# Performance work log

Measured on AMD Instinct MI355X. Metric: run time of the kernel, lower is better.

Reference implementation:

```python
import jax, jax.numpy as jnp
import numpy as np

UP_TIME = 1440.0
UP_DIST = 40.0
LOC_CNT = 100000
LOC_LEN = 131072
H = 256


def setup_inputs() -> dict:
    key = jax.random.key(0)
    ks = jax.random.split(key, 12)
    stdv = 1.0 / np.sqrt(H)
    u = lambda k, shape: jax.random.uniform(k, shape, jnp.float32, -stdv, stdv)
    return {
        "td_upper": jax.random.uniform(ks[0], (LOC_LEN,), jnp.float32),
        "td_lower": jax.random.uniform(ks[1], (LOC_LEN,), jnp.float32),
        "ld_upper": jax.random.uniform(ks[2], (LOC_LEN,), jnp.float32),
        "ld_lower": jax.random.uniform(ks[3], (LOC_LEN,), jnp.float32),
        "loc": jax.random.randint(ks[4], (LOC_LEN,), 0, LOC_CNT, jnp.int32),
        "hx": jax.random.normal(ks[5], (H, 1), jnp.float32),
        "weight_ih": u(ks[6], (H, H)),
        "weight_th_upper": u(ks[7], (H, H)),
        "weight_th_lower": u(ks[8], (H, H)),
        "weight_sh_upper": u(ks[9], (H, H)),
        "weight_sh_lower": u(ks[10], (H, H)),
        "location_weight": u(ks[11], (LOC_CNT, H)),
    }


def reference(td_upper, td_lower, ld_upper, ld_lower, loc, hx,
              weight_ih, weight_th_upper, weight_th_lower,
              weight_sh_upper, weight_sh_lower, location_weight):
    tu = jnp.clip(td_upper, 0.0, UP_TIME)
    tl = jnp.clip(td_lower, 0.0, UP_TIME)
    lu = jnp.clip(ld_upper, 0.0, UP_DIST)
    ll = jnp.clip(ld_lower, 0.0, UP_DIST)

    e = location_weight[loc]  # [L, H] gathered POI embeddings
    # Ttd[i] @ e[i] = (tu[i]*W_tu@e[i] + tl[i]*W_tl@e[i]) / (tu[i]+tl[i])
    a = jnp.einsum('hk,lk->lh', weight_th_upper, e)
    b = jnp.einsum('hk,lk->lh', weight_th_lower, e)
    t = (tu[:, None] * a + tl[:, None] * b) / (tu + tl)[:, None]  # [L, H]
    # Sld[i] @ t[i]
    c = jnp.einsum('hk,lk->lh', weight_sh_upper, t)
    d = jnp.einsum('hk,lk->lh', weight_sh_lower, t)
    s = (lu[:, None] * c + ll[:, None] * d) / (lu + ll)[:, None]  # [L, H]

    loc_vec = jnp.sum(s, axis=0)[:, None]  # [H, 1]
    usr_vec = weight_ih @ hx               # [H, 1]
    return jax.nn.sigmoid(loc_vec + usr_vec)
```

## Files before the change

### kernel.cpp

```cpp
#include <hip/hip_runtime.h>
#include <math.h>

#define H 256
#define TILE 256

__global__ __launch_bounds__(256) void strnn_gather(
    const float* __restrict__ td_u, const float* __restrict__ td_l,
    const float* __restrict__ ld_u, const float* __restrict__ ld_l,
    const int* __restrict__ loc, const float* __restrict__ table,
    float* __restrict__ v, int L)
{
    __shared__ float4 s_w[TILE];
    __shared__ int    s_loc[TILE];
    __shared__ float  s_red[4][4][H];
    const int t    = threadIdx.x;
    const int wave = t >> 6;
    const int lane = t & 63;

    float4 a0 = {0,0,0,0}, a1 = {0,0,0,0}, a2 = {0,0,0,0}, a3 = {0,0,0,0};

    for (int base = blockIdx.x * TILE; base < L; base += gridDim.x * TILE) {
        const int l = base + t;
        const bool ok = (l < L);
        float tu = ok ? fminf(fmaxf(td_u[l], 0.f), 1440.f) : 1.f;
        float tl = ok ? fminf(fmaxf(td_l[l], 0.f), 1440.f) : 1.f;
        float lu = ok ? fminf(fmaxf(ld_u[l], 0.f), 40.f)   : 1.f;
        float ll = ok ? fminf(fmaxf(ld_l[l], 0.f), 40.f)   : 1.f;
        float al = tu / (tu + tl);
        float be = lu / (lu + ll);
        float w0 = be * al, w1 = be * (1.f - al);
        float w2 = (1.f - be) * al, w3 = (1.f - be) * (1.f - al);
        if (!ok) { w0 = w1 = w2 = w3 = 0.f; }
        s_w[t]   = make_float4(w0, w1, w2, w3);
        s_loc[t] = ok ? loc[l] : 0;
        __syncthreads();

        const int r0 = wave * 64;
        #pragma unroll 2
        for (int j = 0; j < 64; j += 8) {
            const float4* addr[8];
            #pragma unroll
            for (int u = 0; u < 8; ++u)
                addr[u] = (const float4*)(table + (size_t)s_loc[r0 + j + u] * H + 4 * lane);
            float4 w[8], e[8];
            #pragma unroll
            for (int u = 0; u < 8; ++u)
                e[u] = *addr[u];
            #pragma unroll
            for (int u = 0; u < 8; ++u)
                w[u] = s_w[r0 + j + u];
            #pragma unroll
            for (int u = 0; u < 8; ++u) {
                a0.x = fmaf(w[u].x, e[u].x, a0.x);
                a0.y = fmaf(w[u].x, e[u].y, a0.y);
                a0.z = fmaf(w[u].x, e[u].z, a0.z);
                a0.w = fmaf(w[u].x, e[u].w, a0.w);
                a1.x = fmaf(w[u].y, e[u].x, a1.x);
                a1.y = fmaf(w[u].y, e[u].y, a1.y);
                a1.z = fmaf(w[u].y, e[u].z, a1.z);
                a1.w = fmaf(w[u].y, e[u].w, a1.w);
                a2.x = fmaf(w[u].z, e[u].x, a2.x);
                a2.y = fmaf(w[u].z, e[u].y, a2.y);
                a2.z = fmaf(w[u].z, e[u].z, a2.z);
                a2.w = fmaf(w[u].z, e[u].w, a2.w);
                a3.x = fmaf(w[u].w, e[u].x, a3.x);
                a3.y = fmaf(w[u].w, e[u].y, a3.y);
                a3.z = fmaf(w[u].w, e[u].z, a3.z);
                a3.w = fmaf(w[u].w, e[u].w, a3.w);
            }
        }
        __syncthreads();
    }

    *(float4*)&s_red[wave][0][4 * lane] = a0;
    *(float4*)&s_red[wave][1][4 * lane] = a1;
    *(float4*)&s_red[wave][2][4 * lane] = a2;
    *(float4*)&s_red[wave][3][4 * lane] = a3;
    __syncthreads();
    #pragma unroll
    for (int c = 0; c < 4; ++c) {
        float s = s_red[0][c][t] + s_red[1][c][t] + s_red[2][c][t] + s_red[3][c][t];
        atomicAdd(&v[c * H + t], s);
    }
}

__global__ __launch_bounds__(256) void strnn_mid(
    const float* __restrict__ Wtu, const float* __restrict__ Wtl,
    const float* __restrict__ Wih, const float* __restrict__ hx,
    const float* __restrict__ v, float* __restrict__ pqu)
{
    const int wave = (blockIdx.x * blockDim.x + threadIdx.x) >> 6;
    const int lane = threadIdx.x & 63;
    const float* v1 = v;
    const float* v2 = v + H;
    const float* v3 = v + 2 * H;
    const float* v4 = v + 3 * H;

    float p = 0.f, q = 0.f, u = 0.f;
    #pragma unroll
    for (int i = 0; i < H; i += 64) {
        const int k = i + lane;
        const float wtu = Wtu[wave * H + k];
        const float wtl = Wtl[wave * H + k];
        p = fmaf(wtu, v1[k], fmaf(wtl, v2[k], p));
        q = fmaf(wtu, v3[k], fmaf(wtl, v4[k], q));
        u = fmaf(Wih[wave * H + k], hx[k], u);
    }
    #pragma unroll
    for (int off = 32; off > 0; off >>= 1) {
        p += __shfl_down(p, off, 64);
        q += __shfl_down(q, off, 64);
        u += __shfl_down(u, off, 64);
    }
    if (lane == 0) {
        pqu[wave]         = p;
        pqu[H + wave]     = q;
        pqu[2 * H + wave] = u;
    }
}

__global__ __launch_bounds__(256) void strnn_out(
    const float* __restrict__ Wsu, const float* __restrict__ Wsl,
    const float* __restrict__ pqu, float* __restrict__ out)
{
    const int wave = (blockIdx.x * blockDim.x + threadIdx.x) >> 6;
    const int lane = threadIdx.x & 63;
    const float* p = pqu;
    const float* q = pqu + H;
    const float* u = pqu + 2 * H;

    float s = 0.f;
    #pragma unroll
    for (int i = 0; i < H; i += 64) {
        const int k = i + lane;
        s = fmaf(Wsu[wave * H + k], p[k], fmaf(Wsl[wave * H + k], q[k], s));
    }
    #pragma unroll
    for (int off = 32; off > 0; off >>= 1)
        s += __shfl_down(s, off, 64);
    if (lane == 0)
        out[wave] = 1.f / (1.f + expf(-(s + u[wave])));
}

extern "C" void kernel_launch(void* const* d_in, const int* in_sizes, int n_in,
                              void* d_out, int out_size, void* d_ws, size_t ws_size,
                              hipStream_t stream) {
    const float* td_u  = (const float*)d_in[0];
    const float* td_l  = (const float*)d_in[1];
    const float* ld_u  = (const float*)d_in[2];
    const float* ld_l  = (const float*)d_in[3];
    const int*   loc   = (const int*)d_in[4];
    const float* hx    = (const float*)d_in[5];
    const float* Wih   = (const float*)d_in[6];
    const float* Wtu   = (const float*)d_in[7];
    const float* Wtl   = (const float*)d_in[8];
    const float* Wsu   = (const float*)d_in[9];
    const float* Wsl   = (const float*)d_in[10];
    const float* table = (const float*)d_in[11];
    const int L = in_sizes[0];

    float* v   = (float*)d_ws;
    float* pqu = v + 4 * H;

    hipMemsetAsync(v, 0, 4 * H * sizeof(float), stream);

    strnn_gather<<<512, 256, 0, stream>>>(td_u, td_l, ld_u, ld_l, loc, table, v, L);
    strnn_mid<<<64, 256, 0, stream>>>(Wtu, Wtl, Wih, hx, v, pqu);
    strnn_out<<<64, 256, 0, stream>>>(Wsu, Wsl, pqu, (float*)d_out);
}
```

Measured before the change: 183.4 us.

## Aggregate per-location weights by scatter, then stream the table in row order

Samples that share a location index are now merged first. A scatter kernel atomically accumulates the four mixing coefficients per sample into a per-location weight buffer. A second kernel then walks the embedding table in row order and accumulates weighted rows. Rows with zero total weight are redirected to row 0, so their distinct loads are skipped. This turns many random 1KB row gathers, including repeats, into near-sequential reads of the touched rows. In exchange it adds a larger workspace memset, contended atomics and an extra kernel launch, and it changes the float summation order.

```diff
diff --git a/kernel.cpp b/kernel.cpp
--- a/kernel.cpp
+++ b/kernel.cpp
@@ -2,74 +2,88 @@
 #include <math.h>
 
 #define H 256
-#define TILE 256
 
-__global__ __launch_bounds__(256) void strnn_gather(
+__global__ __launch_bounds__(256) void strnn_scatter(
     const float* __restrict__ td_u, const float* __restrict__ td_l,
     const float* __restrict__ ld_u, const float* __restrict__ ld_l,
-    const int* __restrict__ loc, const float* __restrict__ table,
-    float* __restrict__ v, int L)
+    const int* __restrict__ loc, float* __restrict__ W, int L)
 {
-    __shared__ float4 s_w[TILE];
-    __shared__ int    s_loc[TILE];
-    __shared__ float  s_red[4][4][H];
+    const int i = blockIdx.x * 256 + threadIdx.x;
+    if (i >= L) return;
+    float tu = fminf(fmaxf(td_u[i], 0.f), 1440.f);
+    float tl = fminf(fmaxf(td_l[i], 0.f), 1440.f);
+    float lu = fminf(fmaxf(ld_u[i], 0.f), 40.f);
+    float ll = fminf(fmaxf(ld_l[i], 0.f), 40.f);
+    float al = tu / (tu + tl);
+    float be = lu / (lu + ll);
+    float* w = W + 4 * (size_t)loc[i];
+    atomicAdd(w + 0, be * al);
+    atomicAdd(w + 1, be * (1.f - al));
+    atomicAdd(w + 2, (1.f - be) * al);
+    atomicAdd(w + 3, (1.f - be) * (1.f - al));
+}
+
+__global__ __launch_bounds__(256) void strnn_stream(
+    const float* __restrict__ table, const float* __restrict__ W,
+    float* __restrict__ v, int R)
+{
+    __shared__ float s_red[4][4][H];
     const int t    = threadIdx.x;
     const int wave = t >> 6;
     const int lane = t & 63;
+    const int gw   = blockIdx.x * 4 + wave;
+    const int nw   = gridDim.x * 4;
 
     float4 a0 = {0,0,0,0}, a1 = {0,0,0,0}, a2 = {0,0,0,0}, a3 = {0,0,0,0};
 
-    for (int base = blockIdx.x * TILE; base < L; base += gridDim.x * TILE) {
-        const int l = base + t;
-        const bool ok = (l < L);
-        float tu = ok ? fminf(fmaxf(td_u[l], 0.f), 1440.f) : 1.f;
-        float tl = ok ? fminf(fmaxf(td_l[l], 0.f), 1440.f) : 1.f;
-        float lu = ok ? fminf(fmaxf(ld_u[l], 0.f), 40.f)   : 1.f;
-        float ll = ok ? fminf(fmaxf(ld_l[l], 0.f), 40.f)   : 1.f;
-        float al = tu / (tu + tl);
-        float be = lu / (lu + ll);
-        float w0 = be * al, w1 = be * (1.f - al);
-        float w2 = (1.f - be) * al, w3 = (1.f - be) * (1.f - al);
-        if (!ok) { w0 = w1 = w2 = w3 = 0.f; }
-        s_w[t]   = make_float4(w0, w1, w2, w3);
-        s_loc[t] = ok ? loc[l] : 0;
-        __syncthreads();
-
-        const int r0 = wave * 64;
-        #pragma unroll 2
-        for (int j = 0; j < 64; j += 8) {
-            const float4* addr[8];
-            #pragma unroll
-            for (int u = 0; u < 8; ++u)
-                addr[u] = (const float4*)(table + (size_t)s_loc[r0 + j + u] * H + 4 * lane);
-            float4 w[8], e[8];
-            #pragma unroll
-            for (int u = 0; u < 8; ++u)
-                e[u] = *addr[u];
-            #pragma unroll
-            for (int u = 0; u < 8; ++u)
-                w[u] = s_w[r0 + j + u];
-            #pragma unroll
-            for (int u = 0; u < 8; ++u) {
-                a0.x = fmaf(w[u].x, e[u].x, a0.x);
-                a0.y = fmaf(w[u].x, e[u].y, a0.y);
-                a0.z = fmaf(w[u].x, e[u].z, a0.z);
-                a0.w = fmaf(w[u].x, e[u].w, a0.w);
-                a1.x = fmaf(w[u].y, e[u].x, a1.x);
-                a1.y = fmaf(w[u].y, e[u].y, a1.y);
-                a1.z = fmaf(w[u].y, e[u].z, a1.z);
-                a1.w = fmaf(w[u].y, e[u].w, a1.w);
-                a2.x = fmaf(w[u].z, e[u].x, a2.x);
-                a2.y = fmaf(w[u].z, e[u].y, a2.y);
-                a2.z = fmaf(w[u].z, e[u].z, a2.z);
-                a2.w = fmaf(w[u].z, e[u].w, a2.w);
-                a3.x = fmaf(w[u].w, e[u].x, a3.x);
-                a3.y = fmaf(w[u].w, e[u].y, a3.y);
-                a3.z = fmaf(w[u].w, e[u].z, a3.z);
-                a3.w = fmaf(w[u].w, e[u].w, a3.w);
-            }
+    for (int base = gw * 8; base + 8 <= R; base += nw * 8) {
+        float4 w[8];
+        #pragma unroll
+        for (int u = 0; u < 8; ++u)
+            w[u] = *(const float4*)(W + 4 * (size_t)(base + u));
+        int ra[8];
+        #pragma unroll
+        for (int u = 0; u < 8; ++u) {
+            float sw = (w[u].x + w[u].y) + (w[u].z + w[u].w);
+            ra[u] = (sw != 0.f) ? (base + u) : 0;
         }
-        __syncthreads();
+        float4 e[8];
+        #pragma unroll
+        for (int u = 0; u < 8; ++u)
+            e[u] = *(const float4*)(table + (size_t)ra[u] * H + 4 * lane);
+        #pragma unroll
+        for (int u = 0; u < 8; ++u) {
+            a0.x = fmaf(w[u].x, e[u].x, a0.x);
+            a0.y = fmaf(w[u].x, e[u].y, a0.y);
+            a0.z = fmaf(w[u].x, e[u].z, a0.z);
+            a0.w = fmaf(w[u].x, e[u].w, a0.w);
+            a1.x = fmaf(w[u].y, e[u].x, a1.x);
+            a1.y = fmaf(w[u].y, e[u].y, a1.y);
+            a1.z = fmaf(w[u].y, e[u].z, a1.z);
+            a1.w = fmaf(w[u].y, e[u].w, a1.w);
+            a2.x = fmaf(w[u].z, e[u].x, a2.x);
+            a2.y = fmaf(w[u].z, e[u].y, a2.y);
+            a2.z = fmaf(w[u].z, e[u].z, a2.z);
+            a2.w = fmaf(w[u].z, e[u].w, a2.w);
+            a3.x = fmaf(w[u].w, e[u].x, a3.x);
+            a3.y = fmaf(w[u].w, e[u].y, a3.y);
+            a3.z = fmaf(w[u].w, e[u].z, a3.z);
+            a3.w = fmaf(w[u].w, e[u].w, a3.w);
+        }
+    }
+    if (gw == 0) {
+        for (int r = R & ~7; r < R; ++r) {
+            float4 w = *(const float4*)(W + 4 * (size_t)r);
+            float4 e = *(const float4*)(table + (size_t)r * H + 4 * lane);
+            a0.x = fmaf(w.x, e.x, a0.x); a0.y = fmaf(w.x, e.y, a0.y);
+            a0.z = fmaf(w.x, e.z, a0.z); a0.w = fmaf(w.x, e.w, a0.w);
+            a1.x = fmaf(w.y, e.x, a1.x); a1.y = fmaf(w.y, e.y, a1.y);
+            a1.z = fmaf(w.y, e.z, a1.z); a1.w = fmaf(w.y, e.w, a1.w);
+            a2.x = fmaf(w.z, e.x, a2.x); a2.y = fmaf(w.z, e.y, a2.y);
+            a2.z = fmaf(w.z, e.z, a2.z); a2.w = fmaf(w.z, e.w, a2.w);
+            a3.x = fmaf(w.w, e.x, a3.x); a3.y = fmaf(w.w, e.y, a3.y);
+            a3.z = fmaf(w.w, e.z, a3.z); a3.w = fmaf(w.w, e.w, a3.w);
+        }
     }
 
     *(float4*)&s_red[wave][0][4 * lane] = a0;
@@ -158,13 +172,16 @@
     const float* Wsl   = (const float*)d_in[10];
     const float* table = (const float*)d_in[11];
     const int L = in_sizes[0];
+    const int R = in_sizes[11] / H;
 
-    float* v   = (float*)d_ws;
+    float* W   = (float*)d_ws;
+    float* v   = W + 4 * (size_t)R;
     float* pqu = v + 4 * H;
 
-    hipMemsetAsync(v, 0, 4 * H * sizeof(float), stream);
+    hipMemsetAsync(W, 0, (4 * (size_t)R + 4 * H) * sizeof(float), stream);
 
-    strnn_gather<<<512, 256, 0, stream>>>(td_u, td_l, ld_u, ld_l, loc, table, v, L);
+    strnn_scatter<<<(L + 255) / 256, 256, 0, stream>>>(td_u, td_l, ld_u, ld_l, loc, W, L);
+    strnn_stream<<<256, 256, 0, stream>>>(table, W, v, R);
     strnn_mid<<<64, 256, 0, stream>>>(Wtu, Wtl, Wih, hx, v, pqu);
     strnn_out<<<64, 256, 0, stream>>>(Wsu, Wsl, pqu, (float*)d_out);
 }
```

New measurement: 231.4 us. 1.26x slower.
